# Performance work log

Measured on AMD Instinct MI355X. Metric: run time of the kernel, lower is better.

Reference implementation:

```python
import jax, jax.numpy as jnp
import numpy as np
from jax import lax

B, C, H, W, S = 2, 64, 32, 32, 16
KS = 5  # conv2 kernel size


def setup_inputs() -> dict:
    key = jax.random.key(0)
    k0, k1, k2 = jax.random.split(key, 3)
    x = jax.random.normal(k0, (B, C, H, W, S), jnp.float32)
    # conv1: 1x1 Conv2d(C -> 3C)
    w1 = jax.random.normal(k1, (3 * C, C, 1, 1), jnp.float32) / np.sqrt(C)
    b1 = jnp.zeros((3 * C,), jnp.float32)
    # conv2: Conv2d(2C -> 1, KSxKS, reflect 'same')
    w2 = jax.random.normal(k2, (1, 2 * C, KS, KS), jnp.float32) / np.sqrt(2 * C * KS * KS)
    b2 = jnp.zeros((1,), jnp.float32)
    return {"x": x, "w1": w1, "b1": b1, "w2": w2, "b2": b2}


def _conv_same_reflect(z, w):
    # z: [N, Cin, H, W], w: [Cout, Cin, k, k]; 'same' with reflect padding
    p = w.shape[-1] // 2
    zp = jnp.pad(z, ((0, 0), (0, 0), (p, p), (p, p)), mode="reflect")
    return lax.conv_general_dilated(zp, w, (1, 1), "VALID",
                                    dimension_numbers=("NCHW", "OIHW", "NCHW"))


def reference(x, w1, b1, w2, b2):
    b, c, h, w, s = x.shape
    # conv1 (1x1) applied per frame == channel mixing einsum
    qkv = jnp.einsum("oc,bchws->bohws", w1[:, :, 0, 0], x) + b1[None, :, None, None, None]
    Q, K, V = jnp.split(qkv, 3, axis=1)  # each [b,c,h,w,s]

    # conv2 on concat(Q[...,s], K[...,t]) is linear in channels:
    # score = conv(Q_s; w2[:, :c]) + conv(K_t; w2[:, c:]) + bias
    def half_score(z, wpart):
        zf = jnp.transpose(z, (0, 4, 1, 2, 3)).reshape(b * s, c, h, w)
        sc = _conv_same_reflect(zf, wpart)[:, 0]  # (b*s, h, w)
        return sc.reshape(b, s, h, w)

    sQ = half_score(Q, w2[:, :c])  # [b, s(query), h, w]
    sK = half_score(K, w2[:, c:])  # [b, t(key),   h, w]

    # score[b,h,w,t,s]
    score = (jnp.transpose(sQ, (0, 2, 3, 1))[:, :, :, None, :]
             + jnp.transpose(sK, (0, 2, 3, 1))[:, :, :, :, None]
             + b2[0])
    attn = jax.nn.softmax(score, axis=-2)  # softmax over key index t
    # V_out[b,c,h,w,s] = sum_t attn[b,h,w,t,s] * V[b,c,h,w,t]
    return jnp.einsum("bhwts,bchwt->bchws", attn, V)
```

## Files before the change

### kernel.cpp

```cpp
#include <hip/hip_runtime.h>


__device__ __forceinline__ int reflect32(int i) {
    if (i < 0) i = -i;
    if (i >= 32) i = 62 - i;
    return i;
}

__global__ void k_fuse(const float* __restrict__ w1, const float* __restrict__ w2,
                       float* __restrict__ Akp) {
    int k  = blockIdx.x;
    int cp = threadIdx.x;
    float acc = 0.f;
    if (k < 25) {
        for (int c = 0; c < 64; ++c)
            acc += w2[(64 + c) * 25 + k] * w1[(64 + c) * 64 + cp];
    }
    Akp[cp * 28 + k] = acc;
}

__global__ void __launch_bounds__(128) k_gemm(const float* __restrict__ x,
                                              const float* __restrict__ Akp,
                                              float* __restrict__ u) {
    int tid  = threadIdx.x;
    int wave = tid >> 6;
    int l    = tid & 63;
    int idx  = blockIdx.x * 64 + l;
    int b    = idx >> 14;
    int pt   = idx & 16383;
    const float* xp = x + b * 1048576 + pt;

    int k0 = __builtin_amdgcn_readfirstlane(wave ? 12 : 0);

    float acc[13];
#pragma unroll
    for (int k = 0; k < 13; ++k) acc[k] = 0.f;

#pragma unroll 4
    for (int c = 0; c < 64; ++c) {
        float xv = xp[c * 16384];
        const float* ak = Akp + c * 28 + k0;
#pragma unroll
        for (int k = 0; k < 13; ++k)
            acc[k] = fmaf(ak[k], xv, acc[k]);
    }

    int kstart = wave ? 1 : 0;
#pragma unroll
    for (int k = 0; k < 13; ++k)
        if (k >= kstart) u[(k0 + k) * 32768 + idx] = acc[k];
}

__global__ void __launch_bounds__(256) k_attn(const float* __restrict__ x,
                                              const float* __restrict__ u,
                                              const float* __restrict__ w1,
                                              const float* __restrict__ b1,
                                              float* __restrict__ out) {
    __shared__ float wT[64 * 65];
    __shared__ float xs[4 * 1040];
    __shared__ float psk[4 * 64];
    __shared__ float sk_s[64];
    __shared__ float ysT[64 * 4];

    int tid = threadIdx.x;
    int g0  = blockIdx.x * 4;
    int b   = g0 >> 10;
    int p0  = g0 & 1023;

    {
        int cc = tid >> 2, sub = tid & 3;
        const float* xbase = x + b * 1048576 + cc * 16384 + p0 * 16 + sub * 4;
#pragma unroll
        for (int pix = 0; pix < 4; ++pix) {
            float4 v = *(const float4*)(xbase + pix * 16);
            float* dst = xs + pix * 1040 + (4 * sub) * 65 + cc;
            dst[0] = v.x; dst[65] = v.y; dst[130] = v.z; dst[195] = v.w;
        }
    }
    for (int e = tid; e < 4096; e += 256)
        wT[(e & 63) * 65 + (e >> 6)] = w1[8192 + e];

    {
        int grp = tid >> 6;
        int pix = (tid >> 4) & 3;
        int t   = tid & 15;
        int p   = p0 + pix;
        int hh  = p >> 5, ww = p & 31;
        int kk0 = grp * 7;
        int nk  = (grp == 3) ? 4 : 7;
        const float* ub = u + b * 16384 + t;
        float acc = 0.f;
        for (int q = 0; q < nk; ++q) {
            int k  = kk0 + q;
            int ky = k / 5, kx = k - ky * 5;
            int rh = reflect32(hh + ky - 2);
            int rw = reflect32(ww + kx - 2);
            acc += ub[k * 32768 + (rh * 32 + rw) * 16];
        }
        psk[grp * 64 + pix * 16 + t] = acc;
    }
    __syncthreads();
    if (tid < 64)
        sk_s[tid] = psk[tid] + psk[64 + tid] + psk[128 + tid] + psk[192 + tid];
    __syncthreads();

    {
        int pix = tid >> 6, cc = tid & 63;
        float sk[16];
#pragma unroll
        for (int t = 0; t < 16; ++t) sk[t] = sk_s[pix * 16 + t];
        float m = sk[0];
#pragma unroll
        for (int t = 1; t < 16; ++t) m = fmaxf(m, sk[t]);
        float e[16], ssum = 0.f;
#pragma unroll
        for (int t = 0; t < 16; ++t) { e[t] = __expf(sk[t] - m); ssum += e[t]; }
        float inv = 1.0f / ssum;

        const float* xr = xs + pix * 1040 + cc;
        float y = 0.f;
#pragma unroll
        for (int t = 0; t < 16; ++t) y = fmaf(e[t], xr[t * 65], y);
        ysT[cc * 4 + pix] = y * inv;
    }
    __syncthreads();

    {
        int cc = tid >> 2, sub = tid & 3;
        float o0 = 0.f, o1 = 0.f, o2 = 0.f, o3 = 0.f;
#pragma unroll
        for (int ii = 0; ii < 16; ++ii) {
            int i = ii * 4 + sub;
            float wv = wT[i * 65 + cc];
            float4 yv = *(const float4*)(ysT + i * 4);
            o0 = fmaf(wv, yv.x, o0);
            o1 = fmaf(wv, yv.y, o1);
            o2 = fmaf(wv, yv.z, o2);
            o3 = fmaf(wv, yv.w, o3);
        }
        o0 += __shfl_xor(o0, 1); o0 += __shfl_xor(o0, 2);
        o1 += __shfl_xor(o1, 1); o1 += __shfl_xor(o1, 2);
        o2 += __shfl_xor(o2, 1); o2 += __shfl_xor(o2, 2);
        o3 += __shfl_xor(o3, 1); o3 += __shfl_xor(o3, 2);
        float bb = b1[128 + cc];
        o0 += bb; o1 += bb; o2 += bb; o3 += bb;

        float* ob = out + (size_t)(b * 64 + cc) * 16384 + p0 * 16 + sub * 4;
        *(float4*)(ob +  0) = make_float4(o0, o0, o0, o0);
        *(float4*)(ob + 16) = make_float4(o1, o1, o1, o1);
        *(float4*)(ob + 32) = make_float4(o2, o2, o2, o2);
        *(float4*)(ob + 48) = make_float4(o3, o3, o3, o3);
    }
}

extern "C" void kernel_launch(void* const* d_in, const int* in_sizes, int n_in,
                              void* d_out, int out_size, void* d_ws, size_t ws_size,
                              hipStream_t stream) {
    const float* x  = (const float*)d_in[0];
    const float* w1 = (const float*)d_in[1];
    const float* b1 = (const float*)d_in[2];
    const float* w2 = (const float*)d_in[3];
    float* out = (float*)d_out;
    float* ws  = (float*)d_ws;

    float* Akp = ws;
    float* u   = ws + 2048;

    k_fuse<<<28, 64, 0, stream>>>(w1, w2, Akp);
    k_gemm<<<512, 128, 0, stream>>>(x, Akp, u);
    k_attn<<<512, 256, 0, stream>>>(x, u, w1, b1, out);
}
```

Before: 88.42 us.

## Split channel reductions across waves and hoist gathers ahead of staging loads

k_fuse now splits its 64-channel reduction across four waves and sums the partials in shared memory. k_gemm changes from two waves splitting the 25 taps to eight waves splitting the 64 channels, which cuts each thread's serial load chain from 64 to 8 and needs a shared-memory cross-wave reduction before writing u. k_attn issues its u gathers into registers before the x and w1 staging loads so their latency overlaps, and loads w1 with float4. The cost is more shared memory and barriers, and k_gemm now uses 25 accumulators per thread.

```diff
diff --git a/kernel.cpp b/kernel.cpp
--- a/kernel.cpp
+++ b/kernel.cpp
@@ -7,48 +7,62 @@
     return i;
 }
 
-__global__ void k_fuse(const float* __restrict__ w1, const float* __restrict__ w2,
-                       float* __restrict__ Akp) {
+__global__ void __launch_bounds__(256) k_fuse(const float* __restrict__ w1,
+                                              const float* __restrict__ w2,
+                                              float* __restrict__ Akp) {
+    __shared__ float part[4][64];
     int k  = blockIdx.x;
-    int cp = threadIdx.x;
+    int w  = __builtin_amdgcn_readfirstlane(threadIdx.x >> 6);
+    int cp = threadIdx.x & 63;
     float acc = 0.f;
-    if (k < 25) {
-        for (int c = 0; c < 64; ++c)
-            acc += w2[(64 + c) * 25 + k] * w1[(64 + c) * 64 + cp];
-    }
-    Akp[cp * 28 + k] = acc;
-}
-
-__global__ void __launch_bounds__(128) k_gemm(const float* __restrict__ x,
+#pragma unroll
+    for (int ci = 0; ci < 16; ++ci) {
+        int c = w * 16 + ci;
+        acc = fmaf(w2[(64 + c) * 25 + k], w1[(64 + c) * 64 + cp], acc);
+    }
+    part[w][cp] = acc;
+    __syncthreads();
+    if (threadIdx.x < 64)
+        Akp[cp * 28 + k] = part[0][cp] + part[1][cp] + part[2][cp] + part[3][cp];
+}
+
+__global__ void __launch_bounds__(512) k_gemm(const float* __restrict__ x,
                                               const float* __restrict__ Akp,
                                               float* __restrict__ u) {
-    int tid  = threadIdx.x;
-    int wave = tid >> 6;
-    int l    = tid & 63;
-    int idx  = blockIdx.x * 64 + l;
-    int b    = idx >> 14;
-    int pt   = idx & 16383;
+    __shared__ float part[8][25][64];
+    int tid = threadIdx.x;
+    int w   = __builtin_amdgcn_readfirstlane(tid >> 6);
+    int l   = tid & 63;
+    int idx = blockIdx.x * 64 + l;
+    int b   = idx >> 14;
+    int pt  = idx & 16383;
     const float* xp = x + b * 1048576 + pt;
 
-    int k0 = __builtin_amdgcn_readfirstlane(wave ? 12 : 0);
-
-    float acc[13];
-#pragma unroll
-    for (int k = 0; k < 13; ++k) acc[k] = 0.f;
-
-#pragma unroll 4
-    for (int c = 0; c < 64; ++c) {
+    float acc[25];
+#pragma unroll
+    for (int k = 0; k < 25; ++k) acc[k] = 0.f;
+
+#pragma unroll
+    for (int ci = 0; ci < 8; ++ci) {
+        int c = w * 8 + ci;
         float xv = xp[c * 16384];
-        const float* ak = Akp + c * 28 + k0;
-#pragma unroll
-        for (int k = 0; k < 13; ++k)
+        const float* ak = Akp + c * 28;
+#pragma unroll
+        for (int k = 0; k < 25; ++k)
             acc[k] = fmaf(ak[k], xv, acc[k]);
     }
-
-    int kstart = wave ? 1 : 0;
-#pragma unroll
-    for (int k = 0; k < 13; ++k)
-        if (k >= kstart) u[(k0 + k) * 32768 + idx] = acc[k];
+#pragma unroll
+    for (int k = 0; k < 25; ++k) part[w][k][l] = acc[k];
+    __syncthreads();
+
+    int base = blockIdx.x * 64;
+    for (int e = tid; e < 1600; e += 512) {
+        int k = e >> 6, l2 = e & 63;
+        float s = part[0][k][l2];
+#pragma unroll
+        for (int ww = 1; ww < 8; ++ww) s += part[ww][k][l2];
+        u[k * 32768 + base + l2] = s;
+    }
 }
 
 __global__ void __launch_bounds__(256) k_attn(const float* __restrict__ x,
@@ -67,6 +81,29 @@
     int b   = g0 >> 10;
     int p0  = g0 & 1023;
 
+    int grp  = __builtin_amdgcn_readfirstlane(tid >> 6);
+    int pixa = (tid >> 4) & 3;
+    int ta   = tid & 15;
+    int nk   = (grp == 3) ? 4 : 7;
+    float ga[7];
+    {
+        int kk0 = grp * 7;
+        int p   = p0 + pixa;
+        int hh  = p >> 5, ww = p & 31;
+        const float* ub = u + b * 16384 + ta;
+#pragma unroll
+        for (int q = 0; q < 7; ++q) {
+            ga[q] = 0.f;
+            if (q < nk) {
+                int k  = kk0 + q;
+                int ky = k / 5, kx = k - ky * 5;
+                int rh = reflect32(hh + ky - 2);
+                int rw = reflect32(ww + kx - 2);
+                ga[q] = ub[k * 32768 + (rh * 32 + rw) * 16];
+            }
+        }
+    }
+
     {
         int cc = tid >> 2, sub = tid & 3;
         const float* xbase = x + b * 1048576 + cc * 16384 + p0 * 16 + sub * 4;
@@ -77,28 +114,21 @@
             dst[0] = v.x; dst[65] = v.y; dst[130] = v.z; dst[195] = v.w;
         }
     }
-    for (int e = tid; e < 4096; e += 256)
-        wT[(e & 63) * 65 + (e >> 6)] = w1[8192 + e];
-
-    {
-        int grp = tid >> 6;
-        int pix = (tid >> 4) & 3;
-        int t   = tid & 15;
-        int p   = p0 + pix;
-        int hh  = p >> 5, ww = p & 31;
-        int kk0 = grp * 7;
-        int nk  = (grp == 3) ? 4 : 7;
-        const float* ub = u + b * 16384 + t;
-        float acc = 0.f;
-        for (int q = 0; q < nk; ++q) {
-            int k  = kk0 + q;
-            int ky = k / 5, kx = k - ky * 5;
-            int rh = reflect32(hh + ky - 2);
-            int rw = reflect32(ww + kx - 2);
-            acc += ub[k * 32768 + (rh * 32 + rw) * 16];
-        }
-        psk[grp * 64 + pix * 16 + t] = acc;
-    }
+    {
+        const float4* w1v4 = (const float4*)(w1 + 8192);
+#pragma unroll
+        for (int j = 0; j < 4; ++j) {
+            int e4 = tid + j * 256;
+            float4 v = w1v4[e4];
+            int c  = e4 >> 4;
+            int i0 = (4 * e4) & 63;
+            float* dst = wT + i0 * 65 + c;
+            dst[0] = v.x; dst[65] = v.y; dst[130] = v.z; dst[195] = v.w;
+        }
+    }
+
+    psk[grp * 64 + pixa * 16 + ta] =
+        ga[0] + ga[1] + ga[2] + ga[3] + ga[4] + ga[5] + ga[6];
     __syncthreads();
     if (tid < 64)
         sk_s[tid] = psk[tid] + psk[64 + tid] + psk[128 + tid] + psk[192 + tid];
@@ -166,7 +196,7 @@
     float* Akp = ws;
     float* u   = ws + 2048;
 
-    k_fuse<<<28, 64, 0, stream>>>(w1, w2, Akp);
-    k_gemm<<<512, 128, 0, stream>>>(x, Akp, u);
+    k_fuse<<<25, 256, 0, stream>>>(w1, w2, Akp);
+    k_gemm<<<512, 512, 0, stream>>>(x, Akp, u);
     k_attn<<<512, 256, 0, stream>>>(x, u, w1, b1, out);
 }
```

Result: faster. 76.32 us (-13.7%).
